# Kernel optimization log

Measured on AMD Instinct MI355X. Metric: run time of the kernel, lower is better.

Reference implementation:

```python
import jax, jax.numpy as jnp
import numpy as np

B, S, H, C = 128, 2048, 1024, 256
N_LANGS = 8


def setup_inputs() -> dict:
    key = jax.random.key(0)
    ks = jax.random.split(key, 7)
    features = jax.random.normal(ks[0], (B, S, H), dtype=jnp.float32)
    language_ids = jax.random.randint(ks[1], (B,), 0, N_LANGS, dtype=jnp.int64)
    attention_mask = jnp.ones((B, S), dtype=jnp.int32)
    # projection MLP params (stored as [in, out]; math-equivalent to torch Linear)
    W1 = jax.random.normal(ks[2], (H, H), dtype=jnp.float32) / np.sqrt(H)
    b1 = jnp.zeros((H,), dtype=jnp.float32)
    W2 = jax.random.normal(ks[3], (H, C), dtype=jnp.float32) / np.sqrt(H)
    b2 = jnp.zeros((C,), dtype=jnp.float32)
    temperature = jnp.array([0.07], dtype=jnp.float32)
    return {"features": features, "W1": W1, "b1": b1, "W2": W2, "b2": b2,
            "temperature": temperature, "language_ids": language_ids,
            "attention_mask": attention_mask}


def reference(features, W1, b1, W2, b2, temperature, language_ids, attention_mask):
    # masked mean pool over seq: [B,S,H] -> [B,H]
    m = attention_mask.astype(features.dtype)[:, :, None]
    pooled = (features * m).sum(axis=1) / m.sum(axis=1)
    # MLP projection head
    h = jax.nn.relu(pooled @ W1 + b1)
    proj = h @ W2 + b2
    # L2 normalize (torch F.normalize eps=1e-12)
    norm = jnp.maximum(jnp.linalg.norm(proj, axis=-1, keepdims=True), 1e-12)
    proj = proj / norm
    # similarity matrix [B,B]
    sim = (proj @ proj.T) / temperature[0]
    # vectorized replacement of the O(B^2) python label loop
    b = language_ids.shape[0]
    diff_lang = language_ids[:, None] != language_ids[None, :]
    off_diag = ~jnp.eye(b, dtype=bool)
    labels = (diff_lang & off_diag).astype(sim.dtype)
    # torch F.cross_entropy with soft (probability) targets:
    # mean over rows of -sum_j labels[i,j] * log_softmax(sim)[i,j]
    logp = jax.nn.log_softmax(sim, axis=-1)
    loss = jnp.mean(-(labels * logp).sum(axis=-1))
    return proj, loss
```

## Files before the change

### kernel.cpp

```cpp
#include <hip/hip_runtime.h>
#include <math.h>

#define BATCH 128
#define SEQ   2048
#define HID   1024
#define CDIM  256
#define SPLIT 16
#define ROWS_PER (SEQ / SPLIT)

typedef float vf4 __attribute__((ext_vector_type(4)));
typedef int   vi4 __attribute__((ext_vector_type(4)));

__global__ __launch_bounds__(256) void pool_partial_kernel(
    const float* __restrict__ feat, const int* __restrict__ mask,
    float* __restrict__ partial)
{
    const int b     = blockIdx.x;
    const int chunk = blockIdx.y;
    const int t     = threadIdx.x;

    const vf4* fp = reinterpret_cast<const vf4*>(feat) +
                    ((size_t)b * SEQ + (size_t)chunk * ROWS_PER) * (HID / 4);
    const vi4* mp = reinterpret_cast<const vi4*>(
                        mask + (size_t)b * SEQ + (size_t)chunk * ROWS_PER);

    vf4 acc = {0.f, 0.f, 0.f, 0.f};
    for (int s = 0; s < ROWS_PER; s += 8) {
        const vi4 m0 = mp[s / 4];
        const vi4 m1 = mp[s / 4 + 1];
        float mm[8];
        mm[0] = (float)m0.x; mm[1] = (float)m0.y; mm[2] = (float)m0.z; mm[3] = (float)m0.w;
        mm[4] = (float)m1.x; mm[5] = (float)m1.y; mm[6] = (float)m1.z; mm[7] = (float)m1.w;
        #pragma unroll
        for (int u = 0; u < 8; ++u) {
            const vf4 v = __builtin_nontemporal_load(&fp[(size_t)(s + u) * (HID / 4) + t]);
            acc += v * mm[u];
        }
    }
    reinterpret_cast<vf4*>(partial)[((size_t)b * SPLIT + chunk) * (HID / 4) + t] = acc;
}

__global__ __launch_bounds__(256) void pool_final_kernel(
    const float* __restrict__ partial, const int* __restrict__ mask,
    float* __restrict__ pooled)
{
    const int b = blockIdx.x;
    const int t = threadIdx.x;

    int local = 0;
    #pragma unroll
    for (int s = t; s < SEQ; s += 256) local += mask[(size_t)b * SEQ + s];
    __shared__ int redi[256];
    redi[t] = local;
    __syncthreads();
    for (int off = 128; off > 0; off >>= 1) {
        if (t < off) redi[t] += redi[t + off];
        __syncthreads();
    }
    const float inv = 1.0f / (float)redi[0];

    vf4 a = {0.f, 0.f, 0.f, 0.f};
    #pragma unroll
    for (int c = 0; c < SPLIT; ++c)
        a += reinterpret_cast<const vf4*>(partial)[((size_t)b * SPLIT + c) * (HID / 4) + t];
    a *= inv;
    reinterpret_cast<vf4*>(pooled)[(size_t)b * (HID / 4) + t] = a;
}

__global__ __launch_bounds__(256) void mlp1_kernel(
    const float* __restrict__ pooled, const float* __restrict__ W1,
    const float* __restrict__ b1, float* __restrict__ hout)
{
    __shared__ float ps[2 * HID];
    const int jc = blockIdx.x;
    const int b0 = blockIdx.y * 2;
    const int t  = threadIdx.x;

    const vf4* src = reinterpret_cast<const vf4*>(pooled + (size_t)b0 * HID);
    vf4* dst = reinterpret_cast<vf4*>(ps);
    #pragma unroll
    for (int i = 0; i < 2; ++i) dst[t + i * 256] = src[t + i * 256];
    __syncthreads();

    const int j = jc * 256 + t;
    float a0 = 0.f, a1 = 0.f;
    for (int k = 0; k < HID; k += 8) {
        float w[8];
        #pragma unroll
        for (int u = 0; u < 8; ++u) w[u] = W1[(size_t)(k + u) * HID + j];
        #pragma unroll
        for (int u = 0; u < 8; ++u) {
            a0 = fmaf(ps[k + u],       w[u], a0);
            a1 = fmaf(ps[HID + k + u], w[u], a1);
        }
    }
    const float bias = b1[j];
    hout[(size_t)b0 * HID + j]       = fmaxf(a0 + bias, 0.f);
    hout[(size_t)(b0 + 1) * HID + j] = fmaxf(a1 + bias, 0.f);
}

__global__ __launch_bounds__(256) void mlp2_norm_kernel(
    const float* __restrict__ hin, const float* __restrict__ W2,
    const float* __restrict__ b2, float* __restrict__ proj)
{
    __shared__ float hs[HID];
    const int b = blockIdx.x;
    const int t = threadIdx.x;

    reinterpret_cast<vf4*>(hs)[t] =
        reinterpret_cast<const vf4*>(hin + (size_t)b * HID)[t];
    __syncthreads();

    float acc = 0.f;
    for (int k = 0; k < HID; k += 8) {
        float w[8];
        #pragma unroll
        for (int u = 0; u < 8; ++u) w[u] = W2[(size_t)(k + u) * CDIM + t];
        #pragma unroll
        for (int u = 0; u < 8; ++u) acc = fmaf(hs[k + u], w[u], acc);
    }
    acc += b2[t];

    __shared__ float red[CDIM];
    red[t] = acc * acc;
    __syncthreads();
    for (int off = CDIM / 2; off > 0; off >>= 1) {
        if (t < off) red[t] += red[t + off];
        __syncthreads();
    }
    const float norm = fmaxf(sqrtf(red[0]), 1e-12f);
    proj[(size_t)b * CDIM + t] = acc / norm;
}

__global__ __launch_bounds__(128) void sim_loss_kernel(
    const float* __restrict__ proj, const float* __restrict__ temp,
    const int* __restrict__ lang, float* __restrict__ loss_part)
{
    const int i = blockIdx.x;
    const int j = threadIdx.x;

    __shared__ float pi[CDIM];
    if (j < CDIM / 4)
        reinterpret_cast<vf4*>(pi)[j] =
            reinterpret_cast<const vf4*>(proj + (size_t)i * CDIM)[j];
    __syncthreads();

    const vf4* pj = reinterpret_cast<const vf4*>(proj + (size_t)j * CDIM);
    float acc = 0.f;
    #pragma unroll 8
    for (int c = 0; c < CDIM / 4; ++c) {
        const vf4 v = pj[c];
        acc = fmaf(pi[4 * c + 0], v.x, acc);
        acc = fmaf(pi[4 * c + 1], v.y, acc);
        acc = fmaf(pi[4 * c + 2], v.z, acc);
        acc = fmaf(pi[4 * c + 3], v.w, acc);
    }
    const float s = acc / temp[0];
    const int li = lang[i];

    __shared__ float r1[BATCH];
    __shared__ int   ci[BATCH];

    r1[j] = s;
    __syncthreads();
    for (int off = BATCH / 2; off > 0; off >>= 1) {
        if (j < off) r1[j] = fmaxf(r1[j], r1[j + off]);
        __syncthreads();
    }
    const float m = r1[0];
    __syncthreads();

    r1[j] = expf(s - m);
    __syncthreads();
    for (int off = BATCH / 2; off > 0; off >>= 1) {
        if (j < off) r1[j] += r1[j + off];
        __syncthreads();
    }
    const float lse = m + logf(r1[0]);
    __syncthreads();

    const bool sel = (lang[j] != li) && (j != i);
    r1[j] = sel ? s : 0.f;
    ci[j] = sel ? 1 : 0;
    __syncthreads();
    for (int off = BATCH / 2; off > 0; off >>= 1) {
        if (j < off) { r1[j] += r1[j + off]; ci[j] += ci[j + off]; }
        __syncthreads();
    }
    if (j == 0) loss_part[i] = (float)ci[0] * lse - r1[0];
}

__global__ __launch_bounds__(128) void loss_reduce_kernel(
    const float* __restrict__ loss_part, float* __restrict__ out)
{
    const int t = threadIdx.x;
    __shared__ float red[BATCH];
    red[t] = loss_part[t];
    __syncthreads();
    for (int off = BATCH / 2; off > 0; off >>= 1) {
        if (t < off) red[t] += red[t + off];
        __syncthreads();
    }
    if (t == 0) out[0] = red[0] / (float)BATCH;
}

extern "C" void kernel_launch(void* const* d_in, const int* in_sizes, int n_in,
                              void* d_out, int out_size, void* d_ws, size_t ws_size,
                              hipStream_t stream)
{
    const float* feat = (const float*)d_in[0];
    const float* W1   = (const float*)d_in[1];
    const float* b1   = (const float*)d_in[2];
    const float* W2   = (const float*)d_in[3];
    const float* b2   = (const float*)d_in[4];
    const float* temp = (const float*)d_in[5];
    const int*   lang = (const int*)d_in[6];
    const int*   amask= (const int*)d_in[7];
    float* out = (float*)d_out;
    float* ws  = (float*)d_ws;

    float* partial   = ws;
    float* pooled    = partial + (size_t)BATCH * SPLIT * HID;
    float* hbuf      = pooled + (size_t)BATCH * HID;
    float* loss_part = hbuf + (size_t)BATCH * HID;

    pool_partial_kernel<<<dim3(BATCH, SPLIT), 256, 0, stream>>>(feat, amask, partial);
    pool_final_kernel<<<BATCH, 256, 0, stream>>>(partial, amask, pooled);
    mlp1_kernel<<<dim3(HID / 256, BATCH / 2), 256, 0, stream>>>(pooled, W1, b1, hbuf);
    mlp2_norm_kernel<<<BATCH, CDIM, 0, stream>>>(hbuf, W2, b2, out);
    sim_loss_kernel<<<BATCH, BATCH, 0, stream>>>(out, temp, lang, loss_part);
    loss_reduce_kernel<<<1, BATCH, 0, stream>>>(loss_part, out + (size_t)BATCH * CDIM);
}
```

Before: 242.2 us.

## Split-K the MLP layers and widen pool-final grid for more parallelism

The first MLP layer is split over 16 K-chunks with 8 batch rows per block, so each W1 load is reused 8 times and the grid grows to 1024 blocks. Partial sums go to a workspace and are reduced, with bias and ReLU applied, inside a new split-K second-layer kernel. That kernel's partials are summed and normalized in a final kernel. Pool-final is spread over 4 column chunks per batch row. This targets low occupancy in the serial MLP kernels, at the cost of one extra launch and extra partial-sum traffic.

```diff
diff --git a/kernel.cpp b/kernel.cpp
--- a/kernel.cpp
+++ b/kernel.cpp
@@ -7,6 +7,8 @@
 #define CDIM  256
 #define SPLIT 16
 #define ROWS_PER (SEQ / SPLIT)
+#define KC1   16
+#define KC2   4
 
 typedef float vf4 __attribute__((ext_vector_type(4)));
 typedef int   vi4 __attribute__((ext_vector_type(4)));
@@ -44,8 +46,9 @@
     const float* __restrict__ partial, const int* __restrict__ mask,
     float* __restrict__ pooled)
 {
-    const int b = blockIdx.x;
-    const int t = threadIdx.x;
+    const int b  = blockIdx.x;
+    const int cc = blockIdx.y;
+    const int t  = threadIdx.x;
 
     int local = 0;
     #pragma unroll
@@ -59,67 +62,96 @@
     }
     const float inv = 1.0f / (float)redi[0];
 
-    vf4 a = {0.f, 0.f, 0.f, 0.f};
+    const int col = cc * 256 + t;
+    float a = 0.f;
     #pragma unroll
     for (int c = 0; c < SPLIT; ++c)
-        a += reinterpret_cast<const vf4*>(partial)[((size_t)b * SPLIT + c) * (HID / 4) + t];
-    a *= inv;
-    reinterpret_cast<vf4*>(pooled)[(size_t)b * (HID / 4) + t] = a;
-}
-
-__global__ __launch_bounds__(256) void mlp1_kernel(
+        a += partial[((size_t)b * SPLIT + c) * HID + col];
+    pooled[(size_t)b * HID + col] = a * inv;
+}
+
+__global__ __launch_bounds__(256) void mlp1_partial_kernel(
     const float* __restrict__ pooled, const float* __restrict__ W1,
-    const float* __restrict__ b1, float* __restrict__ hout)
-{
-    __shared__ float ps[2 * HID];
+    float* __restrict__ part1)
+{
     const int jc = blockIdx.x;
-    const int b0 = blockIdx.y * 2;
+    const int bg = blockIdx.y;
+    const int kc = blockIdx.z;
     const int t  = threadIdx.x;
 
-    const vf4* src = reinterpret_cast<const vf4*>(pooled + (size_t)b0 * HID);
-    vf4* dst = reinterpret_cast<vf4*>(ps);
-    #pragma unroll
-    for (int i = 0; i < 2; ++i) dst[t + i * 256] = src[t + i * 256];
+    __shared__ float ps[8][64];
+    if (t < 128) {
+        const int r = t >> 4;
+        const int c = (t & 15) * 4;
+        *reinterpret_cast<vf4*>(&ps[r][c]) =
+            *reinterpret_cast<const vf4*>(&pooled[(size_t)(bg * 8 + r) * HID + kc * 64 + c]);
+    }
     __syncthreads();
 
     const int j = jc * 256 + t;
-    float a0 = 0.f, a1 = 0.f;
-    for (int k = 0; k < HID; k += 8) {
-        float w[8];
-        #pragma unroll
-        for (int u = 0; u < 8; ++u) w[u] = W1[(size_t)(k + u) * HID + j];
+    const float* w = W1 + (size_t)(kc * 64) * HID + j;
+
+    float acc[8];
+    #pragma unroll
+    for (int r = 0; r < 8; ++r) acc[r] = 0.f;
+
+    #pragma unroll
+    for (int k = 0; k < 64; k += 8) {
+        float wv[8];
+        #pragma unroll
+        for (int u = 0; u < 8; ++u) wv[u] = w[(size_t)(k + u) * HID];
         #pragma unroll
         for (int u = 0; u < 8; ++u) {
-            a0 = fmaf(ps[k + u],       w[u], a0);
-            a1 = fmaf(ps[HID + k + u], w[u], a1);
+            #pragma unroll
+            for (int r = 0; r < 8; ++r)
+                acc[r] = fmaf(ps[r][k + u], wv[u], acc[r]);
         }
     }
-    const float bias = b1[j];
-    hout[(size_t)b0 * HID + j]       = fmaxf(a0 + bias, 0.f);
-    hout[(size_t)(b0 + 1) * HID + j] = fmaxf(a1 + bias, 0.f);
-}
-
-__global__ __launch_bounds__(256) void mlp2_norm_kernel(
-    const float* __restrict__ hin, const float* __restrict__ W2,
-    const float* __restrict__ b2, float* __restrict__ proj)
-{
-    __shared__ float hs[HID];
+    #pragma unroll
+    for (int r = 0; r < 8; ++r)
+        part1[((size_t)kc * BATCH + bg * 8 + r) * HID + j] = acc[r];
+}
+
+__global__ __launch_bounds__(256) void mlp2_partial_kernel(
+    const float* __restrict__ part1, const float* __restrict__ b1,
+    const float* __restrict__ W2, float* __restrict__ part2)
+{
+    const int b  = blockIdx.x;
+    const int kc = blockIdx.y;
+    const int t  = threadIdx.x;
+
+    __shared__ float hs[256];
+    float s = b1[kc * 256 + t];
+    #pragma unroll
+    for (int p = 0; p < KC1; ++p)
+        s += part1[((size_t)p * BATCH + b) * HID + kc * 256 + t];
+    hs[t] = fmaxf(s, 0.f);
+    __syncthreads();
+
+    const float* w = W2 + (size_t)(kc * 256) * CDIM + t;
+    float acc = 0.f;
+    #pragma unroll
+    for (int k = 0; k < 256; k += 8) {
+        float wv[8];
+        #pragma unroll
+        for (int u = 0; u < 8; ++u) wv[u] = w[(size_t)(k + u) * CDIM];
+        #pragma unroll
+        for (int u = 0; u < 8; ++u) acc = fmaf(hs[k + u], wv[u], acc);
+    }
+    part2[((size_t)kc * BATCH + b) * CDIM + t] = acc;
+}
+
+__global__ __launch_bounds__(256) void mlp2_final_kernel(
+    const float* __restrict__ part2, const float* __restrict__ b2,
+    float* __restrict__ proj)
+{
     const int b = blockIdx.x;
     const int t = threadIdx.x;
 
-    reinterpret_cast<vf4*>(hs)[t] =
-        reinterpret_cast<const vf4*>(hin + (size_t)b * HID)[t];
-    __syncthreads();
-
-    float acc = 0.f;
-    for (int k = 0; k < HID; k += 8) {
-        float w[8];
-        #pragma unroll
-        for (int u = 0; u < 8; ++u) w[u] = W2[(size_t)(k + u) * CDIM + t];
-        #pragma unroll
-        for (int u = 0; u < 8; ++u) acc = fmaf(hs[k + u], w[u], acc);
-    }
-    acc += b2[t];
+    float acc = b2[t];
+    #pragma unroll
+    for (int p = 0; p < KC2; ++p)
+        acc += part2[((size_t)p * BATCH + b) * CDIM + t];
 
     __shared__ float red[CDIM];
     red[t] = acc * acc;
@@ -221,13 +253,15 @@
 
     float* partial   = ws;
     float* pooled    = partial + (size_t)BATCH * SPLIT * HID;
-    float* hbuf      = pooled + (size_t)BATCH * HID;
-    float* loss_part = hbuf + (size_t)BATCH * HID;
+    float* part1     = pooled + (size_t)BATCH * HID;
+    float* part2     = part1 + (size_t)KC1 * BATCH * HID;
+    float* loss_part = part2 + (size_t)KC2 * BATCH * CDIM;
 
     pool_partial_kernel<<<dim3(BATCH, SPLIT), 256, 0, stream>>>(feat, amask, partial);
-    pool_final_kernel<<<BATCH, 256, 0, stream>>>(partial, amask, pooled);
-    mlp1_kernel<<<dim3(HID / 256, BATCH / 2), 256, 0, stream>>>(pooled, W1, b1, hbuf);
-    mlp2_norm_kernel<<<BATCH, CDIM, 0, stream>>>(hbuf, W2, b2, out);
+    pool_final_kernel<<<dim3(BATCH, 4), 256, 0, stream>>>(partial, amask, pooled);
+    mlp1_partial_kernel<<<dim3(HID / 256, BATCH / 8, KC1), 256, 0, stream>>>(pooled, W1, part1);
+    mlp2_partial_kernel<<<dim3(BATCH, KC2), 256, 0, stream>>>(part1, b1, W2, part2);
+    mlp2_final_kernel<<<BATCH, CDIM, 0, stream>>>(part2, b2, out);
     sim_loss_kernel<<<BATCH, BATCH, 0, stream>>>(out, temp, lang, loss_part);
     loss_reduce_kernel<<<1, BATCH, 0, stream>>>(loss_part, out + (size_t)BATCH * CDIM);
 }
```

Measured after the change: 206.8 us (median of 2 runs). 14.6% less time.
